# Performance work log

Hardware: AMD Instinct MI355X
Metric: run time of the kernel (lower is better)

The kernel has to match this reference:

```python
import jax, jax.numpy as jnp
import numpy as np

D_MODEL = 1024
NHEAD = 16
D_K = D_MODEL // NHEAD


def setup_inputs() -> dict:
    key = jax.random.key(0)
    ks = jax.random.split(key, 9)
    B, S = 2, 2048
    std = 1.0 / np.sqrt(D_MODEL)
    x = jax.random.normal(ks[0], (B, S, D_MODEL), dtype=jnp.float32)
    Wq = jax.random.uniform(ks[1], (D_MODEL, D_MODEL), jnp.float32, -std, std)
    bq = jax.random.uniform(ks[2], (D_MODEL,), jnp.float32, -std, std)
    Wk = jax.random.uniform(ks[3], (D_MODEL, D_MODEL), jnp.float32, -std, std)
    bk = jax.random.uniform(ks[4], (D_MODEL,), jnp.float32, -std, std)
    Wv = jax.random.uniform(ks[5], (D_MODEL, D_MODEL), jnp.float32, -std, std)
    bv = jax.random.uniform(ks[6], (D_MODEL,), jnp.float32, -std, std)
    Wo = jax.random.uniform(ks[7], (D_MODEL, D_MODEL), jnp.float32, -std, std)
    bo = jax.random.uniform(ks[8], (D_MODEL,), jnp.float32, -std, std)
    return {"x": x, "Wq": Wq, "bq": bq, "Wk": Wk, "bk": bk,
            "Wv": Wv, "bv": bv, "Wo": Wo, "bo": bo}


def reference(x, Wq, bq, Wk, bk, Wv, bv, Wo, bo):
    B, S, _ = x.shape
    scale = jnp.float32(np.sqrt(D_K))
    # Linear layers (torch nn.Linear: y = x @ W.T + b; here W stored as [in,out])
    q = (x @ Wq + bq).reshape(B, S, NHEAD, D_K).transpose(0, 2, 1, 3)  # [B,H,S,Dk]
    k = (x @ Wk + bk).reshape(B, S, NHEAD, D_K).transpose(0, 2, 1, 3)
    v = (x @ Wv + bv).reshape(B, S, NHEAD, D_K).transpose(0, 2, 1, 3)
    scores = jnp.einsum('bhqd,bhkd->bhqk', q, k) / scale  # [B,H,S,S]
    attn = jax.nn.softmax(scores, axis=-1)
    # dropout is identity in eval / deterministic reference
    out = jnp.einsum('bhqk,bhkd->bhqd', attn, v)  # [B,H,S,Dk]
    out = out.transpose(0, 2, 1, 3).reshape(B, S, D_MODEL)
    return out @ Wo + bo
```

## Files before the change

### kernel.cpp

```cpp
#include <hip/hip_runtime.h>
#include <math.h>

#define DM    1024
#define NH    16
#define DK    64
#define SLEN  2048
#define NB    2
#define MROWS (NB*SLEN)
#define QSCALE 0.1803368801111204f

typedef unsigned short u16;
typedef unsigned int   u32;
typedef short  s16x8 __attribute__((ext_vector_type(8)));
typedef __fp16 h16x2 __attribute__((ext_vector_type(2)));
typedef _Float16 f16x8 __attribute__((ext_vector_type(8)));
typedef float  f32x4  __attribute__((ext_vector_type(4)));
typedef float  f32x16 __attribute__((ext_vector_type(16)));

#define MFMA_F16(a,b,c)   __builtin_amdgcn_mfma_f32_16x16x32_f16(a,b,c,0,0,0)
#define MFMA32_F16(a,b,c) __builtin_amdgcn_mfma_f32_32x32x16_f16(a,b,c,0,0,0)

__device__ __forceinline__ void gload16(const void* g, void* l) {
    __builtin_amdgcn_global_load_lds((const __attribute__((address_space(1))) void*)g,
                                     (__attribute__((address_space(3))) void*)l, 16, 0, 0);
}
__device__ __forceinline__ f16x8 as_h(s16x8 v) {
    union { s16x8 s; f16x8 h; } u; u.s = v; return u.h;
}
__device__ __forceinline__ float exp2_hw(float x) {
    float r; asm("v_exp_f32 %0, %1" : "=v"(r) : "v"(x)); return r;
}
__device__ __forceinline__ void pl32swap(u32& a, u32& b) {
    asm volatile("v_permlane32_swap_b32 %0, %1" : "+v"(a), "+v"(b));
}
#define VMCNT0() asm volatile("s_waitcnt vmcnt(0)" ::: "memory")
#define BAR()    __builtin_amdgcn_s_barrier()

__global__ __launch_bounds__(256) void cvt_all(
    const float* __restrict__ x,
    const float* __restrict__ Wq, const float* __restrict__ Wk,
    const float* __restrict__ Wv, const float* __restrict__ Wo,
    _Float16* __restrict__ xh, _Float16* __restrict__ wqkv, _Float16* __restrict__ wo) {
    const int z = blockIdx.z;
    const int t = threadIdx.x;
    if (z == 4) {
        int base = (blockIdx.y * 16 + blockIdx.x) * 256 + t;
#pragma unroll
        for (int u = 0; u < 16; ++u) {
            int i = (base + u * 65536) * 4;
            float4 v = *(const float4*)&x[i];
            float vv[4] = {v.x, v.y, v.z, v.w};
            _Float16 hv[4];
#pragma unroll
            for (int j = 0; j < 4; ++j) hv[j] = (_Float16)vv[j];
            *(ushort4*)&xh[i] = *(ushort4*)hv;
        }
        return;
    }
    __shared__ _Float16 ts[64][72];
    const float* W = (z == 0) ? Wq : (z == 1) ? Wk : (z == 2) ? Wv : Wo;
    _Float16* dst = (z < 3) ? (wqkv + (size_t)z * DM * DM) : wo;
    int k0 = blockIdx.x * 64, n0 = blockIdx.y * 64;
    int kr = t >> 4, c4 = (t & 15) * 4;
#pragma unroll
    for (int u = 0; u < 4; ++u) {
        int k = kr + u * 16;
        float4 v = *(const float4*)&W[(size_t)(k0 + k) * DM + n0 + c4];
        float vv[4] = {v.x, v.y, v.z, v.w};
#pragma unroll
        for (int j = 0; j < 4; ++j) ts[c4 + j][k] = (_Float16)vv[j];
    }
    __syncthreads();
#pragma unroll
    for (int u = 0; u < 4; ++u) {
        int n = kr + u * 16;
        _Float16 hv[4];
#pragma unroll
        for (int j = 0; j < 4; ++j) hv[j] = ts[n][c4 + j];
        *(ushort4*)&dst[(size_t)(n0 + n) * DM + k0 + c4] = *(ushort4*)hv;
    }
}

__global__ __launch_bounds__(256) void gemm_qkv(
    const u16* __restrict__ Ah, const u16* __restrict__ Bt,
    const float* __restrict__ b0, const float* __restrict__ b1, const float* __restrict__ b2,
    _Float16* __restrict__ qf, _Float16* __restrict__ kfp, _Float16* __restrict__ vtp)
{
    __shared__ __align__(16) u16 sAh[2][4096];
    __shared__ __align__(16) u16 sB[2][4096];
    const int tid = threadIdx.x, wid = tid >> 6, lane = tid & 63;
    const int lq = lane & 15, lk = lane >> 4;
    const int wm = wid >> 1, wn = wid & 1;
    const int bm = blockIdx.x * 128, bn = blockIdx.y * 128;

    const f32x4 fz = {0.f, 0.f, 0.f, 0.f};
    f32x4 acc[4][4];
#pragma unroll
    for (int i = 0; i < 4; ++i)
#pragma unroll
        for (int j = 0; j < 4; ++j) acc[i][j] = fz;

    auto stage = [&](int b, int k0) {
#pragma unroll
        for (int u = 0; u < 2; ++u) {
            int idx = u * 256 + tid, row = idx >> 2, c = (idx & 3) ^ ((row >> 1) & 3);
            size_t ga = (size_t)(bm + row) * DM + k0 + c * 8;
            size_t gb = (size_t)(bn + row) * DM + k0 + c * 8;
            int lo = (u * 256 + wid * 64) * 16;
            gload16(Ah + ga, (char*)&sAh[b][0] + lo);
            gload16(Bt + gb, (char*)&sB[b][0] + lo);
        }
    };
    auto compute = [&](int b) {
        s16x8 avh[4], bv[4];
#pragma unroll
        for (int i = 0; i < 4; ++i) {
            int row = wm * 64 + i * 16 + lq;
            int off = row * 32 + ((lk ^ ((row >> 1) & 3)) << 3);
            avh[i] = *(const s16x8*)&sAh[b][off];
        }
#pragma unroll
        for (int j = 0; j < 4; ++j) {
            int row = wn * 64 + j * 16 + lq;
            int off = row * 32 + ((lk ^ ((row >> 1) & 3)) << 3);
            bv[j] = *(const s16x8*)&sB[b][off];
        }
        __builtin_amdgcn_s_setprio(1);
#pragma unroll
        for (int i = 0; i < 4; ++i)
#pragma unroll
            for (int j = 0; j < 4; ++j)
                acc[i][j] = MFMA_F16(as_h(avh[i]), as_h(bv[j]), acc[i][j]);
        __builtin_amdgcn_s_setprio(0);
    };

    int buf = 0;
    stage(0, 0);
    VMCNT0(); BAR();
    for (int t = 0; t < 31; ++t) {
        stage(buf ^ 1, (t + 1) * 32);
        compute(buf);
        VMCNT0(); BAR();
        buf ^= 1;
    }
    compute(buf);

#pragma unroll
    for (int j = 0; j < 4; ++j) {
        int n = bn + wn * 64 + j * 16 + lq;
        int mat = n >> 10, nl = n & 1023;
        int h_ = nl >> 6, d = nl & 63;
        const float* bp = (mat == 0) ? b0 : ((mat == 1) ? b1 : b2);
        float bias = bp[nl];
#pragma unroll
        for (int i = 0; i < 4; ++i) {
            int m0 = bm + wm * 64 + i * 16 + lk * 4;
            int b_ = m0 >> 11, s0 = m0 & (SLEN - 1);
            if (mat == 2) {
                _Float16 v4[4];
#pragma unroll
                for (int r = 0; r < 4; ++r) v4[r] = (_Float16)(acc[i][j][r] + bias);
                *(ushort4*)&vtp[((size_t)(b_ * NH + h_) * DK + d) * SLEN + s0] = *(ushort4*)v4;
            } else {
                _Float16* dst = (mat == 0) ? qf : kfp;
                float sc = (mat == 0) ? QSCALE : 1.0f;
#pragma unroll
                for (int r = 0; r < 4; ++r)
                    dst[((size_t)(b_ * NH + h_) * SLEN + s0 + r) * DK + d] =
                        (_Float16)((acc[i][j][r] + bias) * sc);
            }
        }
    }
}

__global__ __launch_bounds__(256) void gemm_out(
    const u16* __restrict__ Ah, const u16* __restrict__ Bt,
    const float* __restrict__ b0, float* __restrict__ outf)
{
    __shared__ __align__(16) u16 sA[2][128 * 64];
    __shared__ __align__(16) u16 sB[2][64 * 64];
    const int tid = threadIdx.x, wid = tid >> 6, lane = tid & 63;
    const int lq = lane & 15, lk = lane >> 4;
    const int wm = wid >> 1, wn = wid & 1;
    const int bm = blockIdx.x * 128, bn = blockIdx.y * 64;

    const f32x4 fz = {0.f, 0.f, 0.f, 0.f};
    f32x4 acc[4][2];
#pragma unroll
    for (int i = 0; i < 4; ++i)
#pragma unroll
        for (int j = 0; j < 2; ++j) acc[i][j] = fz;

    auto stage = [&](int b, int k0) {
#pragma unroll
        for (int u = 0; u < 4; ++u) {
            int idx = u * 256 + tid, row = idx >> 3, c = (idx & 7) ^ (row & 7);
            gload16(Ah + (size_t)(bm + row) * DM + k0 + c * 8,
                    (char*)&sA[b][0] + (u * 256 + wid * 64) * 16);
        }
#pragma unroll
        for (int u = 0; u < 2; ++u) {
            int idx = u * 256 + tid, row = idx >> 3, c = (idx & 7) ^ (row & 7);
            gload16(Bt + (size_t)(bn + row) * DM + k0 + c * 8,
                    (char*)&sB[b][0] + (u * 256 + wid * 64) * 16);
        }
    };
    auto compute = [&](int b) {
        __builtin_amdgcn_s_setprio(1);
#pragma unroll
        for (int kk = 0; kk < 2; ++kk) {
            s16x8 av[4], bv[2];
#pragma unroll
            for (int i = 0; i < 4; ++i) {
                int row = wm * 64 + i * 16 + lq;
                av[i] = *(const s16x8*)&sA[b][row * 64 + (((kk * 4 + lk) ^ (row & 7)) << 3)];
            }
#pragma unroll
            for (int j = 0; j < 2; ++j) {
                int row = wn * 32 + j * 16 + lq;
                bv[j] = *(const s16x8*)&sB[b][row * 64 + (((kk * 4 + lk) ^ (row & 7)) << 3)];
            }
#pragma unroll
            for (int i = 0; i < 4; ++i)
#pragma unroll
                for (int j = 0; j < 2; ++j)
                    acc[i][j] = MFMA_F16(as_h(av[i]), as_h(bv[j]), acc[i][j]);
        }
        __builtin_amdgcn_s_setprio(0);
    };

    int buf = 0;
    stage(0, 0);
    VMCNT0(); BAR();
    for (int t = 0; t < 15; ++t) {
        stage(buf ^ 1, (t + 1) * 64);
        compute(buf);
        VMCNT0(); BAR();
        buf ^= 1;
    }
    compute(buf);

#pragma unroll
    for (int j = 0; j < 2; ++j) {
        int n = bn + wn * 32 + j * 16 + lq;
        float bias = b0[n];
#pragma unroll
        for (int i = 0; i < 4; ++i)
#pragma unroll
            for (int r = 0; r < 4; ++r) {
                int m = bm + wm * 64 + i * 16 + lk * 4 + r;
                outf[(size_t)m * DM + n] = acc[i][j][r] + bias;
            }
    }
}

__global__ __launch_bounds__(256, 4) void attn_part(
    const _Float16* __restrict__ qf, const _Float16* __restrict__ kf,
    const _Float16* __restrict__ vt,
    _Float16* __restrict__ opart, float* __restrict__ lpart)
{
    __shared__ __align__(16) _Float16 Ks[2][64 * 64], Vs[2][64 * 64];
    const int tid = threadIdx.x, wid = tid >> 6, lane = tid & 63;
    const int ln = lane & 31, l5 = lane >> 5;
    const int phys = blockIdx.x;
    const int virt = (phys & 7) * 128 + (phys >> 3);
    const int bh = virt >> 5, rem = virt & 31;
    const int qb = rem >> 1, half = rem & 1;
    const int qrow = qb * 128 + wid * 32 + ln;
    const int kv0 = half * (SLEN / 2);
    const int NT = (SLEN / 2) / 64;

    f16x8 qv[4];
#pragma unroll
    for (int tp = 0; tp < 4; ++tp)
        qv[tp] = *(const f16x8*)&qf[((size_t)bh * SLEN + qrow) * DK + tp * 16 + l5 * 8];

    const _Float16* kbase = kf + (size_t)bh * SLEN * DK + (size_t)kv0 * DK;
    const _Float16* vbase = vt + (size_t)bh * DK * SLEN + kv0;

    f32x16 O[2];
#pragma unroll
    for (int db = 0; db < 2; ++db)
#pragma unroll
        for (int r = 0; r < 16; ++r) O[db][r] = 0.f;
    float la0 = 0.f, la1 = 0.f, la2 = 0.f, la3 = 0.f;
    const h16x2 ones = {(__fp16)1.0f, (__fp16)1.0f};

    auto stage = [&](int b, int t) {
#pragma unroll
        for (int u = 0; u < 2; ++u) {
            int idx = u * 256 + tid, row = idx >> 3, c = (idx & 7) ^ (row & 7);
            int lo = (u * 256 + wid * 64) * 16;
            gload16(kbase + (size_t)(t * 64 + row) * DK + c * 8, (char*)&Ks[b][0] + lo);
            gload16(vbase + (size_t)row * SLEN + t * 64 + c * 8, (char*)&Vs[b][0] + lo);
        }
    };

    auto compute = [&](int b) {
        f32x16 S[2];
        __builtin_amdgcn_s_setprio(1);
#pragma unroll
        for (int kb = 0; kb < 2; ++kb) {
            f32x16 s;
#pragma unroll
            for (int r = 0; r < 16; ++r) s[r] = 0.f;
            int krow = kb * 32 + ln;
#pragma unroll
            for (int tp = 0; tp < 4; ++tp) {
                int cd = (2 * tp + l5) ^ (krow & 7);
                f16x8 ka = *(const f16x8*)&Ks[b][krow * 64 + cd * 8];
                s = MFMA32_F16(ka, qv[tp], s);
            }
            S[kb] = s;
        }
        __builtin_amdgcn_s_setprio(0);

        u32 pk_[2][8];
#pragma unroll
        for (int kb = 0; kb < 2; ++kb) {
#pragma unroll
            for (int i = 0; i < 8; ++i) {
                float p0 = exp2_hw(S[kb][2 * i]);
                float p1 = exp2_hw(S[kb][2 * i + 1]);
                h16x2 pk = __builtin_amdgcn_cvt_pkrtz(p0, p1);
                switch (i & 3) {
                    case 0: la0 = __builtin_amdgcn_fdot2(pk, ones, la0, false); break;
                    case 1: la1 = __builtin_amdgcn_fdot2(pk, ones, la1, false); break;
                    case 2: la2 = __builtin_amdgcn_fdot2(pk, ones, la2, false); break;
                    default: la3 = __builtin_amdgcn_fdot2(pk, ones, la3, false); break;
                }
                union { h16x2 h; u32 u; } cv; cv.h = pk;
                pk_[kb][i] = cv.u;
            }
            pl32swap(pk_[kb][0], pk_[kb][2]);
            pl32swap(pk_[kb][1], pk_[kb][3]);
            pl32swap(pk_[kb][4], pk_[kb][6]);
            pl32swap(pk_[kb][5], pk_[kb][7]);
        }

        __builtin_amdgcn_s_setprio(1);
#pragma unroll
        for (int kb = 0; kb < 2; ++kb)
#pragma unroll
            for (int t2 = 0; t2 < 2; ++t2) {
                union { u32 w[4]; f16x8 v; } pb;
#pragma unroll
                for (int w = 0; w < 4; ++w) pb.w[w] = pk_[kb][t2 * 4 + w];
#pragma unroll
                for (int db = 0; db < 2; ++db) {
                    int drow = db * 32 + ln;
                    int seg = kb * 2 + t2;
                    int ch = (seg * 2 + l5) ^ (drow & 7);
                    f16x8 va = *(const f16x8*)&Vs[b][drow * 64 + ch * 8];
                    O[db] = MFMA32_F16(va, pb.v, O[db]);
                }
            }
        __builtin_amdgcn_s_setprio(0);
    };

    int buf = 0;
    stage(0, 0);
    VMCNT0(); BAR();
    for (int t = 0; t < NT - 1; ++t) {
        stage(buf ^ 1, t + 1);
        compute(buf);
        VMCNT0(); BAR();
        buf ^= 1;
    }
    compute(buf);

    float lp = (la0 + la1) + (la2 + la3);
    lp += __shfl_xor(lp, 32);
    const int b_ = bh >> 4, h_ = bh & 15;
    const int grow = b_ * SLEN + qrow;
    if (l5 == 0) lpart[((size_t)half * 4096 + grow) * NH + h_] = lp;
    size_t rowbase = ((size_t)half * 4096 + grow) * DM + h_ * 64;
#pragma unroll
    for (int db = 0; db < 2; ++db)
#pragma unroll
        for (int u = 0; u < 4; ++u) {
            int dbase = 8 * u + 4 * l5 + 32 * db;
            _Float16 h4[4];
#pragma unroll
            for (int j = 0; j < 4; ++j) h4[j] = (_Float16)(O[db][4 * u + j]);
            *(ushort4*)&opart[rowbase + dbase] = *(ushort4*)h4;
        }
}

__global__ __launch_bounds__(256) void attn_merge(
    const _Float16* __restrict__ opart, const float* __restrict__ lpart,
    _Float16* __restrict__ aoh)
{
    int idx = blockIdx.x * 256 + threadIdx.x;
    int row = idx >> 7, cq = idx & 127;
    int col = cq * 8, h = col >> 6;
    float l = lpart[(size_t)row * NH + h] + lpart[((size_t)4096 + row) * NH + h];
    float inv = 1.0f / l;
    f16x8 a = *(const f16x8*)&opart[(size_t)row * DM + col];
    f16x8 b = *(const f16x8*)&opart[(size_t)(4096 + row) * DM + col];
    f16x8 o;
#pragma unroll
    for (int j = 0; j < 8; ++j) o[j] = (_Float16)(((float)a[j] + (float)b[j]) * inv);
    *(f16x8*)&aoh[(size_t)row * DM + col] = o;
}

extern "C" void kernel_launch(void* const* d_in, const int* in_sizes, int n_in,
                              void* d_out, int out_size, void* d_ws, size_t ws_size,
                              hipStream_t stream) {
    const float* x  = (const float*)d_in[0];
    const float* Wq = (const float*)d_in[1];
    const float* bq = (const float*)d_in[2];
    const float* Wk = (const float*)d_in[3];
    const float* bk = (const float*)d_in[4];
    const float* Wv = (const float*)d_in[5];
    const float* bv = (const float*)d_in[6];
    const float* Wo = (const float*)d_in[7];
    const float* bo = (const float*)d_in[8];
    float* out = (float*)d_out;

    if (ws_size < (size_t)58 * 1024 * 1024) return;
    char* W = (char*)d_ws;
    _Float16* xh    = (_Float16*)(W);
    _Float16* wqkv  = (_Float16*)(W + ((size_t)8  << 20));
    _Float16* wo    = (_Float16*)(W + ((size_t)14 << 20));
    _Float16* qf    = (_Float16*)(W + ((size_t)16 << 20));
    _Float16* kf    = (_Float16*)(W + ((size_t)24 << 20));
    _Float16* vt    = (_Float16*)(W + ((size_t)32 << 20));
    _Float16* opart = (_Float16*)(W + ((size_t)40 << 20));
    float*    lpart = (float*)(W + ((size_t)57 << 20));
    _Float16* aoh   = xh;

    cvt_all<<<dim3(16, 16, 5), dim3(256), 0, stream>>>(
        x, Wq, Wk, Wv, Wo, xh, wqkv, wo);

    gemm_qkv<<<dim3(32, 24), dim3(256), 0, stream>>>(
        (const u16*)xh, (const u16*)wqkv, bq, bk, bv, qf, kf, vt);

    attn_part<<<dim3(1024), dim3(256), 0, stream>>>(qf, kf, vt, opart, lpart);

    attn_merge<<<dim3(2048), dim3(256), 0, stream>>>(opart, lpart, aoh);

    gemm_out<<<dim3(32, 16), dim3(256), 0, stream>>>(
        (const u16*)aoh, (const u16*)wo, bo, out);
}
```

Measured before the change: 119.0 us.

## Drop split-KV attention and merge kernel, process full KV per block with 128-wide tiles

Attention blocks now iterate over the whole key/value sequence instead of half, and normalize the output directly, removing the partial-output buffers and the separate merge kernel. KV tiles grow from 64 to 128 rows with a 16-way LDS swizzle for V, and launch bounds drop to 2 blocks per SIMD group. This removes the extra global round trip and launch, but halves grid parallelism and doubles LDS and register use per block.

```diff
diff --git a/kernel.cpp b/kernel.cpp
--- a/kernel.cpp
+++ b/kernel.cpp
@@ -254,29 +254,26 @@
     }
 }
 
-__global__ __launch_bounds__(256, 4) void attn_part(
+__global__ __launch_bounds__(256, 2) void attn_mfma(
     const _Float16* __restrict__ qf, const _Float16* __restrict__ kf,
-    const _Float16* __restrict__ vt,
-    _Float16* __restrict__ opart, float* __restrict__ lpart)
+    const _Float16* __restrict__ vt, _Float16* __restrict__ aoh)
 {
-    __shared__ __align__(16) _Float16 Ks[2][64 * 64], Vs[2][64 * 64];
+    __shared__ __align__(16) _Float16 Ks[2][128 * 64];
+    __shared__ __align__(16) _Float16 Vs[2][64 * 128];
     const int tid = threadIdx.x, wid = tid >> 6, lane = tid & 63;
     const int ln = lane & 31, l5 = lane >> 5;
     const int phys = blockIdx.x;
-    const int virt = (phys & 7) * 128 + (phys >> 3);
-    const int bh = virt >> 5, rem = virt & 31;
-    const int qb = rem >> 1, half = rem & 1;
+    const int virt = (phys & 7) * 64 + (phys >> 3);
+    const int bh = virt >> 4, qb = virt & 15;
     const int qrow = qb * 128 + wid * 32 + ln;
-    const int kv0 = half * (SLEN / 2);
-    const int NT = (SLEN / 2) / 64;
 
     f16x8 qv[4];
 #pragma unroll
-    for (int tp = 0; tp < 4; ++tp)
-        qv[tp] = *(const f16x8*)&qf[((size_t)bh * SLEN + qrow) * DK + tp * 16 + l5 * 8];
-
-    const _Float16* kbase = kf + (size_t)bh * SLEN * DK + (size_t)kv0 * DK;
-    const _Float16* vbase = vt + (size_t)bh * DK * SLEN + kv0;
+    for (int t = 0; t < 4; ++t)
+        qv[t] = *(const f16x8*)&qf[((size_t)bh * SLEN + qrow) * DK + t * 16 + l5 * 8];
+
+    const _Float16* kbase = kf + (size_t)bh * SLEN * DK;
+    const _Float16* vbase = vt + (size_t)bh * DK * SLEN;
 
     f32x16 O[2];
 #pragma unroll
@@ -288,19 +285,24 @@
 
     auto stage = [&](int b, int t) {
 #pragma unroll
-        for (int u = 0; u < 2; ++u) {
+        for (int u = 0; u < 4; ++u) {
             int idx = u * 256 + tid, row = idx >> 3, c = (idx & 7) ^ (row & 7);
-            int lo = (u * 256 + wid * 64) * 16;
-            gload16(kbase + (size_t)(t * 64 + row) * DK + c * 8, (char*)&Ks[b][0] + lo);
-            gload16(vbase + (size_t)row * SLEN + t * 64 + c * 8, (char*)&Vs[b][0] + lo);
+            gload16(kbase + (size_t)(t * 128 + row) * DK + c * 8,
+                    (char*)&Ks[b][0] + (u * 256 + wid * 64) * 16);
+        }
+#pragma unroll
+        for (int u = 0; u < 4; ++u) {
+            int idx = u * 256 + tid, row = idx >> 4, c = (idx & 15) ^ (row & 15);
+            gload16(vbase + (size_t)row * SLEN + t * 128 + c * 8,
+                    (char*)&Vs[b][0] + (u * 256 + wid * 64) * 16);
         }
     };
 
     auto compute = [&](int b) {
-        f32x16 S[2];
+        f32x16 S[4];
         __builtin_amdgcn_s_setprio(1);
 #pragma unroll
-        for (int kb = 0; kb < 2; ++kb) {
+        for (int kb = 0; kb < 4; ++kb) {
             f32x16 s;
 #pragma unroll
             for (int r = 0; r < 16; ++r) s[r] = 0.f;
@@ -315,9 +317,9 @@
         }
         __builtin_amdgcn_s_setprio(0);
 
-        u32 pk_[2][8];
-#pragma unroll
-        for (int kb = 0; kb < 2; ++kb) {
+        u32 pk_[4][8];
+#pragma unroll
+        for (int kb = 0; kb < 4; ++kb) {
 #pragma unroll
             for (int i = 0; i < 8; ++i) {
                 float p0 = exp2_hw(S[kb][2 * i]);
@@ -340,7 +342,7 @@
 
         __builtin_amdgcn_s_setprio(1);
 #pragma unroll
-        for (int kb = 0; kb < 2; ++kb)
+        for (int kb = 0; kb < 4; ++kb)
 #pragma unroll
             for (int t2 = 0; t2 < 2; ++t2) {
                 union { u32 w[4]; f16x8 v; } pb;
@@ -349,9 +351,8 @@
 #pragma unroll
                 for (int db = 0; db < 2; ++db) {
                     int drow = db * 32 + ln;
-                    int seg = kb * 2 + t2;
-                    int ch = (seg * 2 + l5) ^ (drow & 7);
-                    f16x8 va = *(const f16x8*)&Vs[b][drow * 64 + ch * 8];
+                    int cd = (kb * 4 + t2 * 2 + l5) ^ (drow & 15);
+                    f16x8 va = *(const f16x8*)&Vs[b][drow * 128 + cd * 8];
                     O[db] = MFMA32_F16(va, pb.v, O[db]);
                 }
             }
@@ -361,7 +362,7 @@
     int buf = 0;
     stage(0, 0);
     VMCNT0(); BAR();
-    for (int t = 0; t < NT - 1; ++t) {
+    for (int t = 0; t < SLEN / 128 - 1; ++t) {
         stage(buf ^ 1, t + 1);
         compute(buf);
         VMCNT0(); BAR();
@@ -371,10 +372,9 @@
 
     float lp = (la0 + la1) + (la2 + la3);
     lp += __shfl_xor(lp, 32);
+    float inv = 1.0f / lp;
     const int b_ = bh >> 4, h_ = bh & 15;
-    const int grow = b_ * SLEN + qrow;
-    if (l5 == 0) lpart[((size_t)half * 4096 + grow) * NH + h_] = lp;
-    size_t rowbase = ((size_t)half * 4096 + grow) * DM + h_ * 64;
+    size_t rowbase = ((size_t)(b_ * SLEN + qrow)) * DM + h_ * 64;
 #pragma unroll
     for (int db = 0; db < 2; ++db)
 #pragma unroll
@@ -382,26 +382,9 @@
             int dbase = 8 * u + 4 * l5 + 32 * db;
             _Float16 h4[4];
 #pragma unroll
-            for (int j = 0; j < 4; ++j) h4[j] = (_Float16)(O[db][4 * u + j]);
-            *(ushort4*)&opart[rowbase + dbase] = *(ushort4*)h4;
-        }
-}
-
-__global__ __launch_bounds__(256) void attn_merge(
-    const _Float16* __restrict__ opart, const float* __restrict__ lpart,
-    _Float16* __restrict__ aoh)
-{
-    int idx = blockIdx.x * 256 + threadIdx.x;
-    int row = idx >> 7, cq = idx & 127;
-    int col = cq * 8, h = col >> 6;
-    float l = lpart[(size_t)row * NH + h] + lpart[((size_t)4096 + row) * NH + h];
-    float inv = 1.0f / l;
-    f16x8 a = *(const f16x8*)&opart[(size_t)row * DM + col];
-    f16x8 b = *(const f16x8*)&opart[(size_t)(4096 + row) * DM + col];
-    f16x8 o;
-#pragma unroll
-    for (int j = 0; j < 8; ++j) o[j] = (_Float16)(((float)a[j] + (float)b[j]) * inv);
-    *(f16x8*)&aoh[(size_t)row * DM + col] = o;
+            for (int j = 0; j < 4; ++j) h4[j] = (_Float16)(O[db][4 * u + j] * inv);
+            *(ushort4*)&aoh[rowbase + dbase] = *(ushort4*)h4;
+        }
 }
 
 extern "C" void kernel_launch(void* const* d_in, const int* in_sizes, int n_in,
@@ -418,17 +401,15 @@
     const float* bo = (const float*)d_in[8];
     float* out = (float*)d_out;
 
-    if (ws_size < (size_t)58 * 1024 * 1024) return;
+    if (ws_size < (size_t)40 * 1024 * 1024) return;
     char* W = (char*)d_ws;
-    _Float16* xh    = (_Float16*)(W);
-    _Float16* wqkv  = (_Float16*)(W + ((size_t)8  << 20));
-    _Float16* wo    = (_Float16*)(W + ((size_t)14 << 20));
-    _Float16* qf    = (_Float16*)(W + ((size_t)16 << 20));
-    _Float16* kf    = (_Float16*)(W + ((size_t)24 << 20));
-    _Float16* vt    = (_Float16*)(W + ((size_t)32 << 20));
-    _Float16* opart = (_Float16*)(W + ((size_t)40 << 20));
-    float*    lpart = (float*)(W + ((size_t)57 << 20));
-    _Float16* aoh   = xh;
+    _Float16* xh   = (_Float16*)(W);
+    _Float16* wqkv = (_Float16*)(W + ((size_t)8  << 20));
+    _Float16* wo   = (_Float16*)(W + ((size_t)14 << 20));
+    _Float16* qf   = (_Float16*)(W + ((size_t)16 << 20));
+    _Float16* kf   = (_Float16*)(W + ((size_t)24 << 20));
+    _Float16* vt   = (_Float16*)(W + ((size_t)32 << 20));
+    _Float16* aoh  = xh;
 
     cvt_all<<<dim3(16, 16, 5), dim3(256), 0, stream>>>(
         x, Wq, Wk, Wv, Wo, xh, wqkv, wo);
@@ -436,9 +417,7 @@
     gemm_qkv<<<dim3(32, 24), dim3(256), 0, stream>>>(
         (const u16*)xh, (const u16*)wqkv, bq, bk, bv, qf, kf, vt);
 
-    attn_part<<<dim3(1024), dim3(256), 0, stream>>>(qf, kf, vt, opart, lpart);
-
-    attn_merge<<<dim3(2048), dim3(256), 0, stream>>>(opart, lpart, aoh);
+    attn_mfma<<<dim3(512), dim3(256), 0, stream>>>(qf, kf, vt, aoh);
 
     gemm_out<<<dim3(32, 16), dim3(256), 0, stream>>>(
         (const u16*)aoh, (const u16*)wo, bo, out);
```

New measurement: 110.9 us. 6.8% less time.
